# Kernel optimization log

Measured on AMD Instinct MI355X. Metric: run time of the kernel, lower is better.

## Reference

```python
import jax, jax.numpy as jnp
import numpy as np

D_MODEL = 1024
NHEAD = 16
D_K = D_MODEL // NHEAD
SPARSITY = 0.9
DROP_P = 0.1


def setup_inputs() -> dict:
    key = jax.random.key(0)
    ks = jax.random.split(key, 11)
    B, S = 4, 2048
    s = 1.0 / np.sqrt(D_MODEL)
    return {
        "query": jax.random.normal(ks[0], (B, S, D_MODEL), jnp.float32),
        "key": jax.random.normal(ks[1], (B, S, D_MODEL), jnp.float32),
        "value": jax.random.normal(ks[2], (B, S, D_MODEL), jnp.float32),
        "Wq": jax.random.normal(ks[3], (D_MODEL, D_MODEL), jnp.float32) * s,
        "bq": jnp.zeros((D_MODEL,), jnp.float32),
        "Wk": jax.random.normal(ks[4], (D_MODEL, D_MODEL), jnp.float32) * s,
        "bk": jnp.zeros((D_MODEL,), jnp.float32),
        "Wv": jax.random.normal(ks[5], (D_MODEL, D_MODEL), jnp.float32) * s,
        "bv": jnp.zeros((D_MODEL,), jnp.float32),
        "Wo": jax.random.normal(ks[6], (D_MODEL, D_MODEL), jnp.float32) * s,
        "bo": jnp.zeros((D_MODEL,), jnp.float32),
    }


def reference(query, key, value, Wq, bq, Wk, bk, Wv, bv, Wo, bo):
    B, S, _ = query.shape
    # torch Linear: x @ W.T + b
    def proj(x, W, b):
        return (x @ W.T + b).reshape(B, S, NHEAD, D_K).transpose(0, 2, 1, 3)

    Q = proj(query, Wq, bq)   # [B,H,S,d_k]
    K = proj(key, Wk, bk)
    V = proj(value, Wv, bv)

    scores = jnp.einsum("bhqd,bhkd->bhqk", Q, K) / jnp.sqrt(jnp.float32(D_K))
    # random sparsity mask: keep where rand > sparsity (fixed RNG key)
    mkey = jax.random.key(42)
    keep = jax.random.uniform(mkey, scores.shape, jnp.float32) > SPARSITY
    scores = jnp.where(keep, scores, -jnp.inf)
    probs = jax.nn.softmax(scores, axis=-1)
    # dropout on attention probs (train mode, inverted dropout)
    dkey = jax.random.key(7)
    dmask = jax.random.bernoulli(dkey, 1.0 - DROP_P, probs.shape)
    probs = probs * dmask / (1.0 - DROP_P)

    out = jnp.einsum("bhqk,bhkd->bhqd", probs, V)  # [B,H,S,d_k]
    out = out.transpose(0, 2, 1, 3).reshape(B, S, D_MODEL)
    return out @ Wo.T + bo
```

## Files before the change

### kernel.cpp

```cpp
#include <hip/hip_runtime.h>
#include <stdint.h>

typedef unsigned short u16;
typedef unsigned int u32;
typedef __attribute__((ext_vector_type(8))) short short8;
typedef __attribute__((ext_vector_type(4))) float f32x4;

#define DEVI static __device__ __forceinline__

#define S_LEN 2048
#define DMODEL 1024
#define NHEAD 16
#define DK 64
#define TH9 7549747u
#define NEG_INF (-__builtin_inff())

DEVI u16 f2bf(float f) {
  u32 u = __builtin_bit_cast(u32, f);
  u32 r = u + 0x7fffu + ((u >> 16) & 1u);
  return (u16)(r >> 16);
}

DEVI short8 cvt8(float4 a, float4 b) {
  short8 r;
  r[0] = (short)f2bf(a.x); r[1] = (short)f2bf(a.y);
  r[2] = (short)f2bf(a.z); r[3] = (short)f2bf(a.w);
  r[4] = (short)f2bf(b.x); r[5] = (short)f2bf(b.y);
  r[6] = (short)f2bf(b.z); r[7] = (short)f2bf(b.w);
  return r;
}

DEVI uint2 threefry(u32 K0, u32 K1, u32 x0, u32 x1) {
  u32 K2 = K0 ^ K1 ^ 0x1BD11BDAu;
#define TFR(r) { x0 += x1; x1 = (x1 << r) | (x1 >> (32 - r)); x1 ^= x0; }
  x0 += K0; x1 += K1;
  TFR(13) TFR(15) TFR(26) TFR(6)  x0 += K1; x1 += K2 + 1u;
  TFR(17) TFR(29) TFR(16) TFR(24) x0 += K2; x1 += K0 + 2u;
  TFR(13) TFR(15) TFR(26) TFR(6)  x0 += K0; x1 += K1 + 3u;
  TFR(17) TFR(29) TFR(16) TFR(24) x0 += K1; x1 += K2 + 4u;
  TFR(13) TFR(15) TFR(26) TFR(6)  x0 += K2; x1 += K0 + 5u;
#undef TFR
  return make_uint2(x0, x1);
}

DEVI u32 tf_bits(u32 key, u32 i) {
  uint2 r = threefry(0u, key, 0u, i);
  return r.x ^ r.y;
}

__global__ __launch_bounds__(256) void rng_kernel(u32* __restrict__ keepw, u32* __restrict__ dropw)
{
  const u32 t = blockIdx.x * 256 + threadIdx.x;
  const u32 q_ = t & 2047u, kth = (t >> 11) & 31u, bh = t >> 16;
  const u32 ibase = (bh * 2048u + q_) * 2048u + kth * 64u;

  u32 kw0 = 0, kw1 = 0;
  #pragma unroll 4
  for (u32 p = 0; p < 32; ++p) {
    kw0 |= (u32)((tf_bits(42u, ibase + p)       >> 9) > TH9) << p;
    kw1 |= (u32)((tf_bits(42u, ibase + 32u + p) >> 9) > TH9) << p;
  }
  u32 dw0 = 0, dw1 = 0, m;
  m = kw0;
  while (m) {
    const u32 p = __builtin_ctz(m); m &= m - 1u;
    dw0 |= (u32)((tf_bits(7u, ibase + p) >> 9) < TH9) << p;
  }
  m = kw1;
  while (m) {
    const u32 p = __builtin_ctz(m); m &= m - 1u;
    dw1 |= (u32)((tf_bits(7u, ibase + 32u + p) >> 9) < TH9) << p;
  }
  *(uint2*)(keepw + 2u * t) = make_uint2(kw0, kw1);
  *(uint2*)(dropw + 2u * t) = make_uint2(dw0, dw1);
}

__global__ __launch_bounds__(256) void proj_kernel(
    const float* __restrict__ Xq, const float* __restrict__ Xk, const float* __restrict__ Xv,
    const float* __restrict__ Wq, const float* __restrict__ Wk, const float* __restrict__ Wv,
    const float* __restrict__ bq, const float* __restrict__ bk, const float* __restrict__ bv,
    u16* __restrict__ Qo, u16* __restrict__ Ko, u16* __restrict__ Vto)
{
  const int z = blockIdx.z;
  const float* X = (z == 0) ? Xq : (z == 1) ? Xk : Xv;
  const float* W = (z == 0) ? Wq : (z == 1) ? Wk : Wv;
  const float* bias = (z == 0) ? bq : (z == 1) ? bk : bv;
  const int m0 = blockIdx.x * 64, n0 = blockIdx.y * 64;
  const int tid = threadIdx.x, w = tid >> 6, lane = tid & 63, l = lane & 15, quad = lane >> 4;

  __shared__ __align__(16) u16 lsA[2048], lsB[2048];

  const int srow = tid >> 2, skp = tid & 3;
  const int sc = ((srow >> 4) * 64 + skp * 16 + (srow & 15)) * 8;
  const float* gA = X + (u32)(m0 + srow) * DMODEL + skp * 8;
  const float* gB = W + (u32)(n0 + srow) * DMODEL + skp * 8;

  f32x4 acc[2][2] = {};
  const int mh = (w >> 1) * 2, nh = (w & 1) * 2;

  for (int k0 = 0; k0 < DMODEL; k0 += 32) {
    short8 av  = cvt8(*(const float4*)(gA + k0), *(const float4*)(gA + k0 + 4));
    short8 bv8 = cvt8(*(const float4*)(gB + k0), *(const float4*)(gB + k0 + 4));
    __syncthreads();
    *(short8*)(lsA + sc) = av;
    *(short8*)(lsB + sc) = bv8;
    __syncthreads();
    short8 a0 = *(const short8*)(lsA + ((mh + 0) * 64 + lane) * 8);
    short8 a1 = *(const short8*)(lsA + ((mh + 1) * 64 + lane) * 8);
    short8 b0 = *(const short8*)(lsB + ((nh + 0) * 64 + lane) * 8);
    short8 b1 = *(const short8*)(lsB + ((nh + 1) * 64 + lane) * 8);
    acc[0][0] = __builtin_amdgcn_mfma_f32_16x16x32_bf16(a0, b0, acc[0][0], 0, 0, 0);
    acc[0][1] = __builtin_amdgcn_mfma_f32_16x16x32_bf16(a0, b1, acc[0][1], 0, 0, 0);
    acc[1][0] = __builtin_amdgcn_mfma_f32_16x16x32_bf16(a1, b0, acc[1][0], 0, 0, 0);
    acc[1][1] = __builtin_amdgcn_mfma_f32_16x16x32_bf16(a1, b1, acc[1][1], 0, 0, 0);
  }

  #pragma unroll
  for (int ma = 0; ma < 2; ++ma) {
    #pragma unroll
    for (int nb = 0; nb < 2; ++nb) {
      const int n = n0 + (nh + nb) * 16 + l;
      const float bval = bias[n];
      const int h = n >> 6, d = n & 63;
      #pragma unroll
      for (int r = 0; r < 4; ++r) {
        const int m = m0 + (mh + ma) * 16 + quad * 4 + r;
        float val = acc[ma][nb][r] + bval;
        if (z == 0) val *= 0.125f;
        const int b = m >> 11, s = m & 2047;
        if (z == 0)      Qo [((u32)(b * NHEAD + h) * S_LEN + s) * DK + d] = f2bf(val);
        else if (z == 1) Ko [((u32)(b * NHEAD + h) * S_LEN + s) * DK + d] = f2bf(val);
        else             Vto[((u32)(b * NHEAD + h) * DK + d) * S_LEN + s] = f2bf(val);
      }
    }
  }
}

__global__ __launch_bounds__(256) void attn_kernel(
    const u16* __restrict__ Qs, const u16* __restrict__ Ks, const u16* __restrict__ Vts,
    const u32* __restrict__ keepw, const u32* __restrict__ dropw,
    u16* __restrict__ ctx)
{
  const int qb = blockIdx.x, bh = blockIdx.y;
  const int tid = threadIdx.x, w = tid >> 6, lane = tid & 63, l = lane & 15, quad = lane >> 4;

  __shared__ __align__(16) u16 Kf[4096];
  __shared__ __align__(16) u16 Vf[4096];
  __shared__ __align__(16) u16 Pf[4][1024];
  __shared__ u32 keepL[128], dropL[128];

  const int qrow0 = qb * 64 + w * 16;
  const u32 qbase = (u32)(bh * S_LEN + qrow0 + l) * DK + quad * 8;
  const short8 qa0 = *(const short8*)(Qs + qbase);
  const short8 qa1 = *(const short8*)(Qs + qbase + 32);

  f32x4 o[4] = {};
  float mr[4] = {NEG_INF, NEG_INF, NEG_INF, NEG_INF};
  float lr[4] = {0.f, 0.f, 0.f, 0.f};

  const int tA = tid, tB = tid + 256;
  const int keyA = tA >> 3, dpA = tA & 7;
  const int kcA = (((dpA >> 2) * 4 + (keyA >> 4)) * 64 + (dpA & 3) * 16 + (keyA & 15)) * 8;
  const u32 gkA = (u32)(bh * S_LEN + keyA) * DK + dpA * 8;
  const int keyB = tB >> 3, dpB = tB & 7;
  const int kcB = (((dpB >> 2) * 4 + (keyB >> 4)) * 64 + (dpB & 3) * 16 + (keyB & 15)) * 8;
  const u32 gkB = (u32)(bh * S_LEN + keyB) * DK + dpB * 8;
  const int vcA = (((keyA >> 4) * 2 + (dpA >> 2)) * 64 + (dpA & 3) * 16 + (keyA & 15)) * 8;
  const u32 gvA = (u32)(bh * DK + keyA) * S_LEN + dpA * 8;
  const int vcB = (((keyB >> 4) * 2 + (dpB >> 2)) * 64 + (dpB & 3) * 16 + (keyB & 15)) * 8;
  const u32 gvB = (u32)(bh * DK + keyB) * S_LEN + dpB * 8;

  for (int kt = 0; kt < 32; ++kt) {
    const u32 ko = (u32)kt * 64u;
    short8 k0v = *(const short8*)(Ks + gkA + ko * DK);
    short8 k1v = *(const short8*)(Ks + gkB + ko * DK);
    short8 v0v = *(const short8*)(Vts + gvA + ko);
    short8 v1v = *(const short8*)(Vts + gvB + ko);
    const u32 mwi = (u32)(bh * 32 + kt) * 4096u + (u32)qb * 128u;
    u32 mw = (tid < 128) ? keepw[mwi + tid] : dropw[mwi + tid - 128];
    __syncthreads();
    *(short8*)(Kf + kcA) = k0v;
    *(short8*)(Kf + kcB) = k1v;
    *(short8*)(Vf + vcA) = v0v;
    *(short8*)(Vf + vcB) = v1v;
    if (tid < 128) keepL[tid] = mw; else dropL[tid - 128] = mw;
    __syncthreads();

    f32x4 sc4[4];
    #pragma unroll
    for (int nc = 0; nc < 4; ++nc) {
      short8 kb0 = *(const short8*)(Kf + (nc * 64 + lane) * 8);
      short8 kb1 = *(const short8*)(Kf + ((4 + nc) * 64 + lane) * 8);
      f32x4 zz = {0.f, 0.f, 0.f, 0.f};
      zz = __builtin_amdgcn_mfma_f32_16x16x32_bf16(qa0, kb0, zz, 0, 0, 0);
      sc4[nc] = __builtin_amdgcn_mfma_f32_16x16x32_bf16(qa1, kb1, zz, 0, 0, 0);
    }

    u16* pw = Pf[w];
    #pragma unroll
    for (int r = 0; r < 4; ++r) {
      const int qq = w * 16 + quad * 4 + r;
      const u32 kwx = keepL[qq * 2], kwy = keepL[qq * 2 + 1];
      const u32 dwx = dropL[qq * 2], dwy = dropL[qq * 2 + 1];
      float v0 = ((kwx >> l) & 1u)        ? sc4[0][r] : NEG_INF;
      float v1 = ((kwx >> (16 + l)) & 1u) ? sc4[1][r] : NEG_INF;
      float v2 = ((kwy >> l) & 1u)        ? sc4[2][r] : NEG_INF;
      float v3 = ((kwy >> (16 + l)) & 1u) ? sc4[3][r] : NEG_INF;
      float mx = fmaxf(fmaxf(v0, v1), fmaxf(v2, v3));
      mx = fmaxf(mx, __shfl_xor(mx, 1));
      mx = fmaxf(mx, __shfl_xor(mx, 2));
      mx = fmaxf(mx, __shfl_xor(mx, 4));
      mx = fmaxf(mx, __shfl_xor(mx, 8));
      const float mn = fmaxf(mr[r], mx);
      const float alpha = (mn == NEG_INF) ? 1.f : __expf(mr[r] - mn);
      mr[r] = mn;
      const float p0 = (v0 == NEG_INF) ? 0.f : __expf(v0 - mn);
      const float p1 = (v1 == NEG_INF) ? 0.f : __expf(v1 - mn);
      const float p2 = (v2 == NEG_INF) ? 0.f : __expf(v2 - mn);
      const float p3 = (v3 == NEG_INF) ? 0.f : __expf(v3 - mn);
      float rs = p0 + p1 + p2 + p3;
      rs += __shfl_xor(rs, 1);
      rs += __shfl_xor(rs, 2);
      rs += __shfl_xor(rs, 4);
      rs += __shfl_xor(rs, 8);
      lr[r] = alpha * lr[r] + rs;
      o[0][r] = o[0][r] * alpha; o[1][r] = o[1][r] * alpha;
      o[2][r] = o[2][r] * alpha; o[3][r] = o[3][r] * alpha;
      const float pd0 = ((dwx >> l) & 1u)        ? p0 * (1.f / 0.9f) : 0.f;
      const float pd1 = ((dwx >> (16 + l)) & 1u) ? p1 * (1.f / 0.9f) : 0.f;
      const float pd2 = ((dwy >> l) & 1u)        ? p2 * (1.f / 0.9f) : 0.f;
      const float pd3 = ((dwy >> (16 + l)) & 1u) ? p3 * (1.f / 0.9f) : 0.f;
      const int hi = l >> 3, bq_ = quad * 4 + r, j = l & 7;
      pw[((hi) * 16 + bq_) * 8 + j]            = f2bf(pd0);
      pw[((2 + hi) * 16 + bq_) * 8 + j]        = f2bf(pd1);
      pw[(64 + hi * 16 + bq_) * 8 + j]         = f2bf(pd2);
      pw[(64 + (2 + hi) * 16 + bq_) * 8 + j]   = f2bf(pd3);
    }
    short8 pa0 = *(const short8*)(Pf[w] + lane * 8);
    short8 pa1 = *(const short8*)(Pf[w] + (64 + lane) * 8);
    #pragma unroll
    for (int nd = 0; nd < 4; ++nd) {
      short8 vb0 = *(const short8*)(Vf + ((nd * 2 + 0) * 64 + lane) * 8);
      short8 vb1 = *(const short8*)(Vf + ((nd * 2 + 1) * 64 + lane) * 8);
      o[nd] = __builtin_amdgcn_mfma_f32_16x16x32_bf16(pa0, vb0, o[nd], 0, 0, 0);
      o[nd] = __builtin_amdgcn_mfma_f32_16x16x32_bf16(pa1, vb1, o[nd], 0, 0, 0);
    }
  }

  const int b = bh >> 4, h = bh & 15;
  #pragma unroll
  for (int r = 0; r < 4; ++r) {
    const float inv = 1.f / lr[r];
    const int qrow = qb * 64 + w * 16 + quad * 4 + r;
    const u32 ob = (u32)(b * S_LEN + qrow) * DMODEL + h * DK;
    ctx[ob + 0  + l] = f2bf(o[0][r] * inv);
    ctx[ob + 16 + l] = f2bf(o[1][r] * inv);
    ctx[ob + 32 + l] = f2bf(o[2][r] * inv);
    ctx[ob + 48 + l] = f2bf(o[3][r] * inv);
  }
}

__global__ __launch_bounds__(256) void oproj_kernel(
    const u16* __restrict__ X, const float* __restrict__ W, const float* __restrict__ bias,
    float* __restrict__ out)
{
  const int m0 = blockIdx.x * 64, n0 = blockIdx.y * 64;
  const int tid = threadIdx.x, w = tid >> 6, lane = tid & 63, l = lane & 15, quad = lane >> 4;

  __shared__ __align__(16) u16 lsA[2048], lsB[2048];

  const int srow = tid >> 2, skp = tid & 3;
  const int sc = ((srow >> 4) * 64 + skp * 16 + (srow & 15)) * 8;
  const u16*  gA = X + (u32)(m0 + srow) * DMODEL + skp * 8;
  const float* gB = W + (u32)(n0 + srow) * DMODEL + skp * 8;

  f32x4 acc[2][2] = {};
  const int mh = (w >> 1) * 2, nh = (w & 1) * 2;

  for (int k0 = 0; k0 < DMODEL; k0 += 32) {
    short8 av  = *(const short8*)(gA + k0);
    short8 bv8 = cvt8(*(const float4*)(gB + k0), *(const float4*)(gB + k0 + 4));
    __syncthreads();
    *(short8*)(lsA + sc) = av;
    *(short8*)(lsB + sc) = bv8;
    __syncthreads();
    short8 a0 = *(const short8*)(lsA + ((mh + 0) * 64 + lane) * 8);
    short8 a1 = *(const short8*)(lsA + ((mh + 1) * 64 + lane) * 8);
    short8 b0 = *(const short8*)(lsB + ((nh + 0) * 64 + lane) * 8);
    short8 b1 = *(const short8*)(lsB + ((nh + 1) * 64 + lane) * 8);
    acc[0][0] = __builtin_amdgcn_mfma_f32_16x16x32_bf16(a0, b0, acc[0][0], 0, 0, 0);
    acc[0][1] = __builtin_amdgcn_mfma_f32_16x16x32_bf16(a0, b1, acc[0][1], 0, 0, 0);
    acc[1][0] = __builtin_amdgcn_mfma_f32_16x16x32_bf16(a1, b0, acc[1][0], 0, 0, 0);
    acc[1][1] = __builtin_amdgcn_mfma_f32_16x16x32_bf16(a1, b1, acc[1][1], 0, 0, 0);
  }

  #pragma unroll
  for (int ma = 0; ma < 2; ++ma) {
    #pragma unroll
    for (int nb = 0; nb < 2; ++nb) {
      const int n = n0 + (nh + nb) * 16 + l;
      const float bval = bias[n];
      #pragma unroll
      for (int r = 0; r < 4; ++r) {
        const int m = m0 + (mh + ma) * 16 + quad * 4 + r;
        out[(u32)m * DMODEL + n] = acc[ma][nb][r] + bval;
      }
    }
  }
}

extern "C" void kernel_launch(void* const* d_in, const int* in_sizes, int n_in,
                              void* d_out, int out_size, void* d_ws, size_t ws_size,
                              hipStream_t stream) {
  (void)in_sizes; (void)n_in; (void)out_size; (void)ws_size;
  const float* q  = (const float*)d_in[0];
  const float* k  = (const float*)d_in[1];
  const float* v  = (const float*)d_in[2];
  const float* Wq = (const float*)d_in[3];
  const float* bq = (const float*)d_in[4];
  const float* Wk = (const float*)d_in[5];
  const float* bk = (const float*)d_in[6];
  const float* Wv = (const float*)d_in[7];
  const float* bv = (const float*)d_in[8];
  const float* Wo = (const float*)d_in[9];
  const float* bo = (const float*)d_in[10];

  char* ws = (char*)d_ws;
  u16* Qs   = (u16*)(ws);
  u16* Ks   = (u16*)(ws + 16777216);
  u16* Vts  = (u16*)(ws + 33554432);
  u16* ctx  = (u16*)(ws + 50331648);
  u32* keepw = (u32*)(ws + 67108864);
  u32* dropw = (u32*)(ws + 100663296);

  rng_kernel<<<dim3(16384), 256, 0, stream>>>(keepw, dropw);
  proj_kernel<<<dim3(128, 16, 3), 256, 0, stream>>>(q, k, v, Wq, Wk, Wv,
                                                    bq, bk, bv, Qs, Ks, Vts);
  attn_kernel<<<dim3(32, 64), 256, 0, stream>>>(Qs, Ks, Vts, keepw, dropw, ctx);
  oproj_kernel<<<dim3(128, 16), 256, 0, stream>>>(ctx, Wo, bo, (float*)d_out);
}
```

Before: 1.300 ms.

## Compact kept indices per wavefront to run dropout RNG without divergence

Reworks the RNG kernel so each lane handles one key position and the keep mask is built with a wavefront ballot. Kept indices are packed into an LDS queue via mbcnt, and the dropout threefry runs on full 64-lane batches instead of per-thread sparse loops that diverge. It also specializes threefry for zero key/counter words, uses native rotates and integer threshold compares, and writes drop bits with atomicOr into a memset-zeroed buffer. The cost is an extra memset and scattered atomics on global memory.

```diff
diff --git a/kernel.cpp b/kernel.cpp
--- a/kernel.cpp
+++ b/kernel.cpp
@@ -3,6 +3,7 @@
 
 typedef unsigned short u16;
 typedef unsigned int u32;
+typedef unsigned long long u64;
 typedef __attribute__((ext_vector_type(8))) short short8;
 typedef __attribute__((ext_vector_type(4))) float f32x4;
 
@@ -12,8 +13,9 @@
 #define DMODEL 1024
 #define NHEAD 16
 #define DK 64
-#define TH9 7549747u
 #define NEG_INF (-__builtin_inff())
+#define KEEPC 3865470976u
+#define DROPC 3865470464u
 
 DEVI u16 f2bf(float f) {
   u32 u = __builtin_bit_cast(u32, f);
@@ -30,49 +32,61 @@
   return r;
 }
 
-DEVI uint2 threefry(u32 K0, u32 K1, u32 x0, u32 x1) {
-  u32 K2 = K0 ^ K1 ^ 0x1BD11BDAu;
-#define TFR(r) { x0 += x1; x1 = (x1 << r) | (x1 >> (32 - r)); x1 ^= x0; }
-  x0 += K0; x1 += K1;
-  TFR(13) TFR(15) TFR(26) TFR(6)  x0 += K1; x1 += K2 + 1u;
-  TFR(17) TFR(29) TFR(16) TFR(24) x0 += K2; x1 += K0 + 2u;
-  TFR(13) TFR(15) TFR(26) TFR(6)  x0 += K0; x1 += K1 + 3u;
-  TFR(17) TFR(29) TFR(16) TFR(24) x0 += K1; x1 += K2 + 4u;
-  TFR(13) TFR(15) TFR(26) TFR(6)  x0 += K2; x1 += K0 + 5u;
+DEVI u32 tf_bits(u32 key, u32 i) {
+  const u32 K2 = key ^ 0x1BD11BDAu;
+  u32 x0 = 0u, x1 = i + key;
+#define TFR(r) { x0 += x1; x1 = __builtin_rotateleft32(x1, r); x1 ^= x0; }
+  TFR(13) TFR(15) TFR(26) TFR(6)  x0 += key; x1 += K2 + 1u;
+  TFR(17) TFR(29) TFR(16) TFR(24) x0 += K2;  x1 += 2u;
+  TFR(13) TFR(15) TFR(26) TFR(6)    x1 += key + 3u;
+  TFR(17) TFR(29) TFR(16) TFR(24) x0 += key; x1 += K2 + 4u;
+  TFR(13) TFR(15) TFR(26) TFR(6)  x0 += K2;  x1 += 5u;
 #undef TFR
-  return make_uint2(x0, x1);
-}
-
-DEVI u32 tf_bits(u32 key, u32 i) {
-  uint2 r = threefry(0u, key, 0u, i);
-  return r.x ^ r.y;
+  return x0 ^ x1;
+}
+
+DEVI u32 mbcnt64(u64 m) {
+  return __builtin_amdgcn_mbcnt_hi((u32)(m >> 32),
+         __builtin_amdgcn_mbcnt_lo((u32)m, 0u));
 }
 
 __global__ __launch_bounds__(256) void rng_kernel(u32* __restrict__ keepw, u32* __restrict__ dropw)
 {
-  const u32 t = blockIdx.x * 256 + threadIdx.x;
-  const u32 q_ = t & 2047u, kth = (t >> 11) & 31u, bh = t >> 16;
-  const u32 ibase = (bh * 2048u + q_) * 2048u + kth * 64u;
-
-  u32 kw0 = 0, kw1 = 0;
-  #pragma unroll 4
-  for (u32 p = 0; p < 32; ++p) {
-    kw0 |= (u32)((tf_bits(42u, ibase + p)       >> 9) > TH9) << p;
-    kw1 |= (u32)((tf_bits(42u, ibase + 32u + p) >> 9) > TH9) << p;
-  }
-  u32 dw0 = 0, dw1 = 0, m;
-  m = kw0;
-  while (m) {
-    const u32 p = __builtin_ctz(m); m &= m - 1u;
-    dw0 |= (u32)((tf_bits(7u, ibase + p) >> 9) < TH9) << p;
-  }
-  m = kw1;
-  while (m) {
-    const u32 p = __builtin_ctz(m); m &= m - 1u;
-    dw1 |= (u32)((tf_bits(7u, ibase + 32u + p) >> 9) < TH9) << p;
-  }
-  *(uint2*)(keepw + 2u * t) = make_uint2(kw0, kw1);
-  *(uint2*)(dropw + 2u * t) = make_uint2(dw0, dw1);
+  __shared__ u32 qbuf[4][128];
+  const int wv = threadIdx.x >> 6, lane = threadIdx.x & 63;
+  const u32 W = blockIdx.x * 4u + (u32)wv;
+  const u32 q0 = (W & 31u) * 64u, kth = (W >> 5) & 31u, bh = W >> 10;
+
+  u32 ivar = (bh * 2048u + q0) * 2048u + kth * 64u + (u32)lane;
+  u32 widx = (bh * 32u + kth) * 4096u + q0 * 2u;
+  u32 wpos = 0, rpos = 0;
+
+  for (int g = 0; g < 64; ++g) {
+    const u32 bits = tf_bits(42u, ivar);
+    const bool kept = (bits >= KEEPC);
+    const u64 keep = __ballot(kept);
+    if (lane == 0) *(uint2*)(keepw + widx) = make_uint2((u32)keep, (u32)(keep >> 32));
+    const u32 before = mbcnt64(keep);
+    if (kept) qbuf[wv][(wpos + before) & 127u] = ivar;
+    wpos += (u32)__popcll(keep);
+    if (wpos - rpos >= 64u) {
+      const u32 idx = qbuf[wv][(rpos + (u32)lane) & 127u];
+      const u32 db = tf_bits(7u, idx);
+      const u32 kk = idx & 2047u, qq = (idx >> 11) & 2047u, bb = idx >> 22;
+      const u32 word = (bb * 32u + (kk >> 6)) * 4096u + qq * 2u + ((kk >> 5) & 1u);
+      if (db < DROPC) atomicOr(dropw + word, 1u << (kk & 31u));
+      rpos += 64u;
+    }
+    ivar += 2048u; widx += 2u;
+  }
+  const u32 rem = wpos - rpos;
+  if ((u32)lane < rem) {
+    const u32 idx = qbuf[wv][(rpos + (u32)lane) & 127u];
+    const u32 db = tf_bits(7u, idx);
+    const u32 kk = idx & 2047u, qq = (idx >> 11) & 2047u, bb = idx >> 22;
+    const u32 word = (bb * 32u + (kk >> 6)) * 4096u + qq * 2u + ((kk >> 5) & 1u);
+    if (db < DROPC) atomicOr(dropw + word, 1u << (kk & 31u));
+  }
 }
 
 __global__ __launch_bounds__(256) void proj_kernel(
@@ -333,6 +347,7 @@
   u32* keepw = (u32*)(ws + 67108864);
   u32* dropw = (u32*)(ws + 100663296);
 
+  hipMemsetAsync(dropw, 0, 33554432, stream);
   rng_kernel<<<dim3(16384), 256, 0, stream>>>(keepw, dropw);
   proj_kernel<<<dim3(128, 16, 3), 256, 0, stream>>>(q, k, v, Wq, Wk, Wv,
                                                     bq, bk, bv, Qs, Ks, Vts);
```

New measurement: 1.391 ms. 7.0% more time.
